# Kernel tuning notes

Measured on AMD Instinct MI355X. Metric: run time of the kernel, lower is better.

## Reference

```python
import jax, jax.numpy as jnp
import numpy as np

L, B, D_IN, D = 96, 32, 4, 128   # leaves, batch, input feats, dim_feedforward
NB, NC = 3, 6                    # n_blocks, n_classes
E = L * (L - 1)                  # directed edges, no self-loops


def _adjacency():
    # one-hot receiver/sender matrices, shape (E, L)
    pairs = np.array([(i, j) for i in range(L) for j in range(L) if i != j])
    recv, send = pairs[:, 0], pairs[:, 1]
    rr = np.zeros((E, L), np.float32); rr[np.arange(E), recv] = 1.0
    rs = np.zeros((E, L), np.float32); rs[np.arange(E), send] = 1.0
    return rr, rs


def setup_inputs() -> dict:
    key = jax.random.key(0)
    ks = jax.random.split(key, 24)
    rr, rs = _adjacency()
    inp = {
        'inputs': jax.random.normal(ks[0], (L, B, D_IN), jnp.float32),
        'rel_rec': jnp.broadcast_to(jnp.asarray(rr), (B, E, L)),
        'rel_send': jnp.broadcast_to(jnp.asarray(rs), (B, E, L)),
    }
    s = 0.1
    # initial MLP: D_IN -> D -> D
    inp['W0a'] = s * jax.random.normal(ks[1], (D_IN, D)); inp['b0a'] = jnp.zeros((D,))
    inp['W0b'] = s * jax.random.normal(ks[2], (D, D));    inp['b0b'] = jnp.zeros((D,))
    # per-block edge MLP (2D -> D -> D) and node MLP (D -> D -> D), stacked over NB
    inp['eW1'] = s * jax.random.normal(ks[3], (NB, 2 * D, D)); inp['eb1'] = jnp.zeros((NB, D))
    inp['eW2'] = s * jax.random.normal(ks[4], (NB, D, D));     inp['eb2'] = jnp.zeros((NB, D))
    inp['nW1'] = s * jax.random.normal(ks[5], (NB, D, D));     inp['nb1'] = jnp.zeros((NB, D))
    inp['nW2'] = s * jax.random.normal(ks[6], (NB, D, D));     inp['nb2'] = jnp.zeros((NB, D))
    # final MLP: 2D -> D -> NC
    inp['fW1'] = s * jax.random.normal(ks[7], (2 * D, D)); inp['fb1'] = jnp.zeros((D,))
    inp['fW2'] = s * jax.random.normal(ks[8], (D, NC));    inp['fb2'] = jnp.zeros((NC,))
    return inp


def _mlp(x, W1, b1, W2, b2):
    return jax.nn.elu(jax.nn.elu(x @ W1 + b1) @ W2 + b2)


def reference(inputs, rel_rec, rel_send, W0a, b0a, W0b, b0b,
              eW1, eb1, eW2, eb2, nW1, nb1, nW2, nb2,
              fW1, fb1, fW2, fb2):
    def node2edge(h):
        # (b,l,d) -> (b,E,2d): cat([senders, receivers])
        senders = jnp.einsum('bel,bld->bed', rel_send, h)
        receivers = jnp.einsum('bel,bld->bed', rel_rec, h)
        return jnp.concatenate([senders, receivers], axis=2)

    def edge2node(h):
        # (b,E,d) -> (b,l,d), mean over incoming edges
        incoming = jnp.einsum('bel,bed->bld', rel_rec, h)
        denom = rel_rec.sum(1)[:, 1]  # (b,)
        return incoming / denom[:, None, None]

    x = jnp.transpose(inputs, (1, 0, 2))           # (b, l, d_in)
    x = _mlp(x, W0a, b0a, W0b, b0b)                # (b, l, D)
    x = node2edge(x)                               # (b, E, 2D)
    for i in range(NB):
        x = _mlp(x, eW1[i], eb1[i], eW2[i], eb2[i])  # (b, E, D)
        x = edge2node(x)                             # (b, l, D)
        x = _mlp(x, nW1[i], nb1[i], nW2[i], nb2[i])  # (b, l, D)
        x = node2edge(x)                             # (b, E, 2D)
    out = jax.nn.elu(x @ fW1 + fb1) @ fW2 + fb2    # (b, E, NC)
    return out
```

## Files before the change

kernel.cpp:

```cpp
#include <hip/hip_runtime.h>
#include <hip/hip_bf16.h>

#define LN 96
#define BN 32
#define DM 128
#define EPN 95

typedef __attribute__((ext_vector_type(8))) short s16x8;
typedef __attribute__((ext_vector_type(4))) float f32x4;

__device__ __forceinline__ float eluf(float x){ return x > 0.f ? x : __expf(x) - 1.f; }
__device__ __forceinline__ unsigned short f2bf(float f){
    unsigned u = __float_as_uint(f);
    return (unsigned short)((u + 0x7fff + ((u >> 16) & 1)) >> 16);
}
__device__ __forceinline__ float bf2f(unsigned short h){ return __uint_as_float(((unsigned)h) << 16); }
__device__ __forceinline__ unsigned cvtpk(float lo, float hi){
    unsigned r;
    asm("v_cvt_pk_bf16_f32 %0, %1, %2" : "=v"(r) : "v"(lo), "v"(hi));
    return r;
}

struct SrcTab { const float* p[19]; };

__global__ void conv_pack_kernel(SrcTab tab, unsigned short* __restrict__ hi,
                                 unsigned short* __restrict__ lo){
    int tid = blockIdx.x * 256 + threadIdx.x;
    int m = tid >> 11, c = tid & 2047;
    int l = c & 63, f = c >> 6;
    int n = (f >> 2) * 16 + (l & 15);
    int k0 = (f & 3) * 32 + (l >> 4) * 8;
    union { unsigned short us[8]; uint4 v; } ph, pl;
#pragma unroll
    for (int e = 0; e < 8; ++e){
        float x;
        if (m == 18) x = (n < 6) ? tab.p[18][(k0 + e) * 6 + n] : 0.f;
        else         x = tab.p[m][(k0 + e) * DM + n];
        unsigned short h = f2bf(x);
        ph.us[e] = h;
        pl.us[e] = f2bf(x - bf2f(h));
    }
    *(uint4*)(hi + (size_t)tid * 8) = ph.v;
    *(uint4*)(lo + (size_t)tid * 8) = pl.v;
}

__device__ __forceinline__ void mmw(const char* atile, int l,
                                    const unsigned short* __restrict__ whW,
                                    const unsigned short* __restrict__ wlW,
                                    f32x4 acc[2]) {
    const int l15 = l & 15, kgrp = l >> 4;
    s16x8 a[4];
#pragma unroll
    for (int ks = 0; ks < 4; ++ks)
        a[ks] = *(const s16x8*)(atile + ((l15 * 256 + (ks * 32 + kgrp * 8) * 2) ^ ((l15 & 7) << 4)));
#pragma unroll
    for (int ntl = 0; ntl < 2; ++ntl) {
#pragma unroll
        for (int ks = 0; ks < 4; ++ks) {
            s16x8 bh = *(const s16x8*)(whW + (size_t)((ntl * 4 + ks) * 64 + l) * 8);
            acc[ntl] = __builtin_amdgcn_mfma_f32_16x16x32_bf16(a[ks], bh, acc[ntl], 0, 0, 0);
        }
#pragma unroll
        for (int ks = 0; ks < 4; ++ks) {
            s16x8 bl = *(const s16x8*)(wlW + (size_t)((ntl * 4 + ks) * 64 + l) * 8);
            acc[ntl] = __builtin_amdgcn_mfma_f32_16x16x32_bf16(a[ks], bl, acc[ntl], 0, 0, 0);
        }
    }
}

__device__ __forceinline__ void store_act(char* atile, int l, int w, f32x4 acc[2]) {
    const int l15 = l & 15, kgrp = l >> 4;
#pragma unroll
    for (int ntl = 0; ntl < 2; ++ntl)
#pragma unroll
        for (int i = 0; i < 4; ++i) {
            int row = kgrp * 4 + i;
            int col = (2 * w + ntl) * 16 + l15;
            *(unsigned short*)(atile + ((row * 256 + col * 2) ^ ((row & 7) << 4))) = f2bf(eluf(acc[ntl][i]));
        }
}

__global__ __launch_bounds__(256) void node0_kernel(
    const float* __restrict__ in,
    const float* __restrict__ W0a, const float* __restrict__ b0a,
    const unsigned short* __restrict__ w2h, const unsigned short* __restrict__ w2l,
    const float* __restrict__ b2,
    const unsigned short* __restrict__ wsh, const unsigned short* __restrict__ wsl,
    const unsigned short* __restrict__ wrh, const unsigned short* __restrict__ wrl,
    const float* __restrict__ bp,
    float* __restrict__ hs, float* __restrict__ hr) {
    __shared__ char atile[16 * 256];
    const int t = threadIdx.x;
    const int q = blockIdx.x >> 5, bblk = blockIdx.x & 31;
    const int row0 = bblk * LN + q * 16;
    const int l = t & 63, w = t >> 6;
    const int l15 = l & 15, kgrp = l >> 4;

    {
        int rr = t >> 4, qq = t & 15, c0 = qq * 8;
        int swz = (rr & 7) << 4;
        union { unsigned short us[8]; uint4 v; } pk;
        int row = row0 + rr;
        int b = row / LN, ll = row - b * LN;
        float4 x = *(const float4*)(in + (size_t)(ll * BN + b) * 4);
#pragma unroll
        for (int j = 0; j < 8; ++j) {
            int cc = c0 + j;
            float a = b0a[cc] + x.x * W0a[cc] + x.y * W0a[DM + cc]
                    + x.z * W0a[2 * DM + cc] + x.w * W0a[3 * DM + cc];
            pk.us[j] = f2bf(eluf(a));
        }
        *(uint4*)(atile + ((rr * 256 + c0 * 2) ^ swz)) = pk.v;
    }
    __syncthreads();

    f32x4 acc[2];
    const int cA = (2 * w) * 16 + l15, cB = (2 * w + 1) * 16 + l15;
    {
        float ba = b2[cA], bb = b2[cB];
        acc[0] = (f32x4){ba, ba, ba, ba};
        acc[1] = (f32x4){bb, bb, bb, bb};
        mmw(atile, l, w2h + w * 4096, w2l + w * 4096, acc);
        __syncthreads();
        store_act(atile, l, w, acc);
        __syncthreads();
    }
    acc[0] = (f32x4){0.f, 0.f, 0.f, 0.f};
    acc[1] = (f32x4){0.f, 0.f, 0.f, 0.f};
    mmw(atile, l, wsh + w * 4096, wsl + w * 4096, acc);
#pragma unroll
    for (int ntl = 0; ntl < 2; ++ntl)
#pragma unroll
        for (int i = 0; i < 4; ++i)
            hs[(size_t)(row0 + kgrp * 4 + i) * DM + (2 * w + ntl) * 16 + l15] = acc[ntl][i];
    {
        float ba = bp[cA], bb = bp[cB];
        acc[0] = (f32x4){ba, ba, ba, ba};
        acc[1] = (f32x4){bb, bb, bb, bb};
        mmw(atile, l, wrh + w * 4096, wrl + w * 4096, acc);
    }
#pragma unroll
    for (int ntl = 0; ntl < 2; ++ntl)
#pragma unroll
        for (int i = 0; i < 4; ++i)
            hr[(size_t)(row0 + kgrp * 4 + i) * DM + (2 * w + ntl) * 16 + l15] = acc[ntl][i];
}

__global__ __launch_bounds__(256) void edge_node_kernel(
    const float* __restrict__ hsIn, const float* __restrict__ hrIn,
    const unsigned short* __restrict__ whi, const unsigned short* __restrict__ wlo,
    int eslot, const float* __restrict__ eb2v,
    int s1, int s2, int sS,
    const float* __restrict__ b1, const float* __restrict__ b2, const float* __restrict__ bp,
    float* __restrict__ hsOut, float* __restrict__ hrOut) {
    __shared__ char y1[LN * 256];
    __shared__ float hrL[6 * DM];
    __shared__ float gL[6 * DM];
    __shared__ char actA[16 * 256];
    __shared__ char actB[16 * 256];
    const int blk = blockIdx.x;
    const int rg = blk >> 5, b = blk & 31;
    const int r0 = rg * 6;
    const int t = threadIdx.x;
    const int w = t >> 6, l = t & 63;
    const int l15 = l & 15, kgrp = l >> 4;

    if (t < 192) {
        int rr = t >> 5, c4 = (t & 31) * 4;
        *(float4*)(hrL + rr * DM + c4) = *(const float4*)(hrIn + ((size_t)(b * LN + r0 + rr)) * DM + c4);
    }
    s16x8 bfr[2][4];
#pragma unroll
    for (int ntl = 0; ntl < 2; ++ntl)
#pragma unroll
        for (int ks = 0; ks < 4; ++ks)
            bfr[ntl][ks] = *(const s16x8*)(whi + (size_t)eslot * 16384 +
                           (size_t)(((2 * w + ntl) * 4 + ks) * 64 + l) * 8);
    float b20 = eb2v[(2 * w) * 16 + l15], b21 = eb2v[(2 * w + 1) * 16 + l15];
    __syncthreads();

    const float* hsB = hsIn + (size_t)(b * LN) * DM;
    for (int rr6 = 0; rr6 < 6; ++rr6) {
        int r = r0 + rr6;
#pragma unroll
        for (int ch = 0; ch < 3; ++ch) {
            float4 h0[2], h1[2];
            int rrs[2], c0s[2];
#pragma unroll
            for (int k = 0; k < 2; ++k) {
                int task = t + (ch * 2 + k) * 256;
                int rr = task >> 4, c0 = (task & 15) * 8;
                rrs[k] = rr; c0s[k] = c0;
                if (rr < EPN) {
                    int j = rr + (rr >= r);
                    const float* hp = hsB + (size_t)j * DM + c0;
                    h0[k] = *(const float4*)hp;
                    h1[k] = *(const float4*)(hp + 4);
                }
            }
#pragma unroll
            for (int k = 0; k < 2; ++k) {
                int rr = rrs[k], c0 = c0s[k];
                int swz = (rr & 7) << 4;
                uint4 pk = make_uint4(0, 0, 0, 0);
                if (rr < EPN) {
                    const float* rp = hrL + rr6 * DM + c0;
                    f32x4 v0 = *(const f32x4*)rp, v1 = *(const f32x4*)(rp + 4);
                    float e0 = eluf(h0[k].x + v0[0]), e1 = eluf(h0[k].y + v0[1]);
                    float e2 = eluf(h0[k].z + v0[2]), e3 = eluf(h0[k].w + v0[3]);
                    float e4 = eluf(h1[k].x + v1[0]), e5 = eluf(h1[k].y + v1[1]);
                    float e6 = eluf(h1[k].z + v1[2]), e7 = eluf(h1[k].w + v1[3]);
                    pk.x = cvtpk(e0, e1); pk.y = cvtpk(e2, e3);
                    pk.z = cvtpk(e4, e5); pk.w = cvtpk(e6, e7);
                }
                *(uint4*)(y1 + ((rr * 256 + c0 * 2) ^ swz)) = pk;
            }
        }
        __syncthreads();
        f32x4 acc[6][2] = {};
#pragma unroll
        for (int mt = 0; mt < 6; ++mt) {
            int arow = mt * 16 + l15;
            const char* rb = y1 + arow * 256;
            int swz = (arow & 7) << 4;
#pragma unroll
            for (int ks = 0; ks < 4; ++ks) {
                s16x8 a = *(const s16x8*)(rb + (((ks * 32 + kgrp * 8) * 2) ^ swz));
                acc[mt][0] = __builtin_amdgcn_mfma_f32_16x16x32_bf16(a, bfr[0][ks], acc[mt][0], 0, 0, 0);
                acc[mt][1] = __builtin_amdgcn_mfma_f32_16x16x32_bf16(a, bfr[1][ks], acc[mt][1], 0, 0, 0);
            }
        }
        float cs0 = 0.f, cs1 = 0.f;
#pragma unroll
        for (int mt = 0; mt < 6; ++mt)
#pragma unroll
            for (int i = 0; i < 4; ++i) {
                int row = mt * 16 + kgrp * 4 + i;
                if (row < EPN) {
                    cs0 += eluf(acc[mt][0][i] + b20);
                    cs1 += eluf(acc[mt][1][i] + b21);
                }
            }
        cs0 += __shfl_xor(cs0, 16); cs0 += __shfl_xor(cs0, 32);
        cs1 += __shfl_xor(cs1, 16); cs1 += __shfl_xor(cs1, 32);
        if (l < 16) {
            gL[rr6 * DM + (2 * w) * 16 + l]     = cs0 * (1.f / 95.f);
            gL[rr6 * DM + (2 * w + 1) * 16 + l] = cs1 * (1.f / 95.f);
        }
        __syncthreads();
    }

    {
        int rr = t >> 4, q = t & 15, c0 = q * 8;
        int swz = (rr & 7) << 4;
        union { unsigned short us[8]; uint4 v; } pk;
        if (rr < 6) {
            const float* src = gL + rr * DM + c0;
            float4 f0 = *(const float4*)(src);
            float4 f1 = *(const float4*)(src + 4);
            pk.us[0] = f2bf(f0.x); pk.us[1] = f2bf(f0.y); pk.us[2] = f2bf(f0.z); pk.us[3] = f2bf(f0.w);
            pk.us[4] = f2bf(f1.x); pk.us[5] = f2bf(f1.y); pk.us[6] = f2bf(f1.z); pk.us[7] = f2bf(f1.w);
        } else pk.v = make_uint4(0, 0, 0, 0);
        *(uint4*)(actA + ((rr * 256 + c0 * 2) ^ swz)) = pk.v;
    }
    __syncthreads();

    f32x4 acc[2];
    const int cA = (2 * w) * 16 + l15, cB = (2 * w + 1) * 16 + l15;
    {
        float ba = b1[cA], bb = b1[cB];
        acc[0] = (f32x4){ba, ba, ba, ba};
        acc[1] = (f32x4){bb, bb, bb, bb};
        mmw(actA, l, whi + (size_t)s1 * 16384 + w * 4096, wlo + (size_t)s1 * 16384 + w * 4096, acc);
        __syncthreads();
        store_act(actB, l, w, acc);
        __syncthreads();
    }
    {
        float ba = b2[cA], bb = b2[cB];
        acc[0] = (f32x4){ba, ba, ba, ba};
        acc[1] = (f32x4){bb, bb, bb, bb};
        mmw(actB, l, whi + (size_t)s2 * 16384 + w * 4096, wlo + (size_t)s2 * 16384 + w * 4096, acc);
        __syncthreads();
        store_act(actA, l, w, acc);
        __syncthreads();
    }
    acc[0] = (f32x4){0.f, 0.f, 0.f, 0.f};
    acc[1] = (f32x4){0.f, 0.f, 0.f, 0.f};
    mmw(actA, l, whi + (size_t)sS * 16384 + w * 4096, wlo + (size_t)sS * 16384 + w * 4096, acc);
#pragma unroll
    for (int ntl = 0; ntl < 2; ++ntl)
#pragma unroll
        for (int i = 0; i < 4; ++i) {
            int row = kgrp * 4 + i;
            if (row < 6)
                hsOut[(size_t)(b * LN + r0 + row) * DM + (2 * w + ntl) * 16 + l15] = acc[ntl][i];
        }
    {
        float ba = bp[cA], bb = bp[cB];
        acc[0] = (f32x4){ba, ba, ba, ba};
        acc[1] = (f32x4){bb, bb, bb, bb};
        mmw(actA, l, whi + (size_t)(sS + 1) * 16384 + w * 4096, wlo + (size_t)(sS + 1) * 16384 + w * 4096, acc);
    }
#pragma unroll
    for (int ntl = 0; ntl < 2; ++ntl)
#pragma unroll
        for (int i = 0; i < 4; ++i) {
            int row = kgrp * 4 + i;
            if (row < 6)
                hrOut[(size_t)(b * LN + r0 + row) * DM + (2 * w + ntl) * 16 + l15] = acc[ntl][i];
        }
}

__global__ void final_kernel(const float* __restrict__ hs, const float* __restrict__ hr,
                             const float* __restrict__ fW2, const float* __restrict__ fb2,
                             float* __restrict__ out) {
    __shared__ float w2l[DM * 6];
    __shared__ float hrbuf[DM];
    const int b = blockIdx.x, r = blockIdx.y;
    const int t = threadIdx.x;
    hrbuf[t] = hr[((size_t)b * LN + r) * DM + t];
    for (int c = 0; c < 6; ++c) w2l[t * 6 + c] = fW2[t * 6 + c];
    __syncthreads();
    int k = t;
    if (k < EPN) {
        int j = k + (k >= r);
        const float* src = hs + ((size_t)b * LN + j) * DM;
        float acc[6];
        for (int c = 0; c < 6; ++c) acc[c] = fb2[c];
        for (int d0 = 0; d0 < DM; d0 += 4) {
            float4 f = *(const float4*)(src + d0);
            float v0 = eluf(f.x + hrbuf[d0 + 0]);
            float v1 = eluf(f.y + hrbuf[d0 + 1]);
            float v2 = eluf(f.z + hrbuf[d0 + 2]);
            float v3 = eluf(f.w + hrbuf[d0 + 3]);
            for (int c = 0; c < 6; ++c)
                acc[c] += v0 * w2l[(d0 + 0) * 6 + c] + v1 * w2l[(d0 + 1) * 6 + c]
                        + v2 * w2l[(d0 + 2) * 6 + c] + v3 * w2l[(d0 + 3) * 6 + c];
        }
        float* o = out + (((size_t)b * (LN * EPN)) + r * EPN + k) * 6;
        for (int c = 0; c < 6; ++c) o[c] = acc[c];
    }
}

extern "C" void kernel_launch(void* const* d_in, const int* in_sizes, int n_in,
                              void* d_out, int out_size, void* d_ws, size_t ws_size,
                              hipStream_t stream) {
    const float* inputs = (const float*)d_in[0];
    const float* W0a = (const float*)d_in[3];
    const float* b0a = (const float*)d_in[4];
    const float* W0b = (const float*)d_in[5];
    const float* b0b = (const float*)d_in[6];
    const float* eW1 = (const float*)d_in[7];
    const float* eb1 = (const float*)d_in[8];
    const float* eW2 = (const float*)d_in[9];
    const float* eb2 = (const float*)d_in[10];
    const float* nW1 = (const float*)d_in[11];
    const float* nb1 = (const float*)d_in[12];
    const float* nW2 = (const float*)d_in[13];
    const float* nb2 = (const float*)d_in[14];
    const float* fW1 = (const float*)d_in[15];
    const float* fb1 = (const float*)d_in[16];
    const float* fW2 = (const float*)d_in[17];
    const float* fb2 = (const float*)d_in[18];
    float* out = (float*)d_out;

    const int NR = BN * LN;
    unsigned short* whi = (unsigned short*)d_ws;
    unsigned short* wlo = whi + 19 * 16384;
    float* hsA = (float*)(wlo + 19 * 16384);
    float* hrA = hsA + NR * DM;
    float* hsB = hrA + NR * DM;
    float* hrB = hsB + NR * DM;

    SrcTab tab;
    tab.p[0] = eW2;          tab.p[1] = eW2 + 16384;  tab.p[2] = eW2 + 32768;
    tab.p[3] = W0b;
    tab.p[4] = eW1;          tab.p[5] = eW1 + 16384;
    tab.p[6] = nW1;          tab.p[7] = nW2;          tab.p[8] = eW1 + 32768;  tab.p[9]  = eW1 + 49152;
    tab.p[10] = nW1 + 16384; tab.p[11] = nW2 + 16384; tab.p[12] = eW1 + 65536; tab.p[13] = eW1 + 81920;
    tab.p[14] = nW1 + 32768; tab.p[15] = nW2 + 32768; tab.p[16] = fW1;         tab.p[17] = fW1 + 16384;
    tab.p[18] = fW2;

    #define WM(m) (whi + (m) * 16384), (wlo + (m) * 16384)

    conv_pack_kernel<<<152, 256, 0, stream>>>(tab, whi, wlo);
    node0_kernel<<<192, 256, 0, stream>>>(inputs, W0a, b0a, WM(3), b0b, WM(4), WM(5), eb1, hsA, hrA);
    edge_node_kernel<<<512, 256, 0, stream>>>(hsA, hrA, whi, wlo, 0, eb2,
                                              6, 7, 8, nb1, nb2, eb1 + DM, hsB, hrB);
    edge_node_kernel<<<512, 256, 0, stream>>>(hsB, hrB, whi, wlo, 1, eb2 + DM,
                                              10, 11, 12, nb1 + DM, nb2 + DM, eb1 + 2 * DM, hsA, hrA);
    edge_node_kernel<<<512, 256, 0, stream>>>(hsA, hrA, whi, wlo, 2, eb2 + 2 * DM,
                                              14, 15, 16, nb1 + 2 * DM, nb2 + 2 * DM, fb1, hsB, hrB);
    final_kernel<<<dim3(BN, LN), 128, 0, stream>>>(hsB, hrB, fW2, fb2, out);
    #undef WM
}
```

Before: 128.8 us.

## Rewrite final edge-MLP output layer as bf16 MFMA over LDS-staged edge tiles

The final kernel now computes the ELU(hs+hr) @ fW2 projection with 16x16x32 bf16 MFMA instructions. It uses split hi/lo bf16 weights from the packed weight buffer, which approximates fp32 precision. Each block handles one batch and six receiver rows. It stages swizzled bf16 activation tiles in LDS, two receivers at a time, instead of one thread per edge doing scalar FMAs with LDS weight reads. This removes the scalar per-thread inner loop at the cost of rounding activations to bf16 and using more LDS per block.

```diff
diff --git a/kernel.cpp b/kernel.cpp
--- a/kernel.cpp
+++ b/kernel.cpp
@@ -312,34 +312,103 @@
         }
 }
 
-__global__ void final_kernel(const float* __restrict__ hs, const float* __restrict__ hr,
-                             const float* __restrict__ fW2, const float* __restrict__ fb2,
-                             float* __restrict__ out) {
-    __shared__ float w2l[DM * 6];
-    __shared__ float hrbuf[DM];
-    const int b = blockIdx.x, r = blockIdx.y;
+__global__ __launch_bounds__(256) void final_kernel(
+    const float* __restrict__ hs, const float* __restrict__ hr,
+    const unsigned short* __restrict__ wfh, const unsigned short* __restrict__ wfl,
+    const float* __restrict__ fb2, float* __restrict__ out) {
+    __shared__ char tA[LN * 256];
+    __shared__ char tB[LN * 256];
+    __shared__ float hrL[6 * DM];
+    const int blk = blockIdx.x;
+    const int rg = blk >> 5, b = blk & 31;
+    const int r0 = rg * 6;
     const int t = threadIdx.x;
-    hrbuf[t] = hr[((size_t)b * LN + r) * DM + t];
-    for (int c = 0; c < 6; ++c) w2l[t * 6 + c] = fW2[t * 6 + c];
+    const int w = t >> 6, l = t & 63;
+    const int l15 = l & 15, kgrp = l >> 4;
+
+    if (t < 192) {
+        int rr = t >> 5, c4 = (t & 31) * 4;
+        *(float4*)(hrL + rr * DM + c4) = *(const float4*)(hr + ((size_t)(b * LN + r0 + rr)) * DM + c4);
+    }
+    s16x8 fh[4], fl4[4];
+#pragma unroll
+    for (int ks = 0; ks < 4; ++ks) {
+        fh[ks]  = *(const s16x8*)(wfh + (size_t)(ks * 64 + l) * 8);
+        fl4[ks] = *(const s16x8*)(wfl + (size_t)(ks * 64 + l) * 8);
+    }
+    float fbv = (l15 < 6) ? fb2[l15] : 0.f;
     __syncthreads();
-    int k = t;
-    if (k < EPN) {
-        int j = k + (k >= r);
-        const float* src = hs + ((size_t)b * LN + j) * DM;
-        float acc[6];
-        for (int c = 0; c < 6; ++c) acc[c] = fb2[c];
-        for (int d0 = 0; d0 < DM; d0 += 4) {
-            float4 f = *(const float4*)(src + d0);
-            float v0 = eluf(f.x + hrbuf[d0 + 0]);
-            float v1 = eluf(f.y + hrbuf[d0 + 1]);
-            float v2 = eluf(f.z + hrbuf[d0 + 2]);
-            float v3 = eluf(f.w + hrbuf[d0 + 3]);
-            for (int c = 0; c < 6; ++c)
-                acc[c] += v0 * w2l[(d0 + 0) * 6 + c] + v1 * w2l[(d0 + 1) * 6 + c]
-                        + v2 * w2l[(d0 + 2) * 6 + c] + v3 * w2l[(d0 + 3) * 6 + c];
-        }
-        float* o = out + (((size_t)b * (LN * EPN)) + r * EPN + k) * 6;
-        for (int c = 0; c < 6; ++c) o[c] = acc[c];
+
+    const float* hsB = hs + (size_t)(b * LN) * DM;
+    for (int pr = 0; pr < 3; ++pr) {
+        const int rA = r0 + pr * 2, rB = rA + 1;
+#pragma unroll
+        for (int ch = 0; ch < 6; ++ch) {
+            float4 h0[2], h1[2];
+            int rrs[2], c0s[2], tts[2];
+#pragma unroll
+            for (int k = 0; k < 2; ++k) {
+                int task = t + (ch * 2 + k) * 256;
+                int tt = task >= 1536;
+                int rem = task - tt * 1536;
+                int rr = rem >> 4, c0 = (rem & 15) * 8;
+                rrs[k] = rr; c0s[k] = c0; tts[k] = tt;
+                if (rr < EPN) {
+                    int r = tt ? rB : rA;
+                    int j = rr + (rr >= r);
+                    const float* hp = hsB + (size_t)j * DM + c0;
+                    h0[k] = *(const float4*)hp;
+                    h1[k] = *(const float4*)(hp + 4);
+                }
+            }
+#pragma unroll
+            for (int k = 0; k < 2; ++k) {
+                int rr = rrs[k], c0 = c0s[k], tt = tts[k];
+                int swz = (rr & 7) << 4;
+                uint4 pk = make_uint4(0, 0, 0, 0);
+                if (rr < EPN) {
+                    const float* rp = hrL + (pr * 2 + tt) * DM + c0;
+                    f32x4 v0 = *(const f32x4*)rp, v1 = *(const f32x4*)(rp + 4);
+                    float e0 = eluf(h0[k].x + v0[0]), e1 = eluf(h0[k].y + v0[1]);
+                    float e2 = eluf(h0[k].z + v0[2]), e3 = eluf(h0[k].w + v0[3]);
+                    float e4 = eluf(h1[k].x + v1[0]), e5 = eluf(h1[k].y + v1[1]);
+                    float e6 = eluf(h1[k].z + v1[2]), e7 = eluf(h1[k].w + v1[3]);
+                    pk.x = cvtpk(e0, e1); pk.y = cvtpk(e2, e3);
+                    pk.z = cvtpk(e4, e5); pk.w = cvtpk(e6, e7);
+                }
+                *(uint4*)((tt ? tB : tA) + ((rr * 256 + c0 * 2) ^ swz)) = pk;
+            }
+        }
+        __syncthreads();
+        for (int q = w; q < 12; q += 4) {
+            int tt = q >= 6;
+            int mt = q - tt * 6;
+            const char* tile = tt ? tB : tA;
+            int r = tt ? rB : rA;
+            int arow = mt * 16 + l15;
+            const char* rb = tile + arow * 256;
+            int swz = (arow & 7) << 4;
+            s16x8 a[4];
+#pragma unroll
+            for (int ks = 0; ks < 4; ++ks)
+                a[ks] = *(const s16x8*)(rb + (((ks * 32 + kgrp * 8) * 2) ^ swz));
+            f32x4 acc = (f32x4){fbv, fbv, fbv, fbv};
+#pragma unroll
+            for (int ks = 0; ks < 4; ++ks)
+                acc = __builtin_amdgcn_mfma_f32_16x16x32_bf16(a[ks], fh[ks], acc, 0, 0, 0);
+#pragma unroll
+            for (int ks = 0; ks < 4; ++ks)
+                acc = __builtin_amdgcn_mfma_f32_16x16x32_bf16(a[ks], fl4[ks], acc, 0, 0, 0);
+            if (l15 < 6) {
+                float* ob = out + ((size_t)b * (LN * EPN) + (size_t)r * EPN) * 6;
+#pragma unroll
+                for (int i = 0; i < 4; ++i) {
+                    int row = mt * 16 + kgrp * 4 + i;
+                    if (row < EPN) ob[(size_t)row * 6 + l15] = acc[i];
+                }
+            }
+        }
+        __syncthreads();
     }
 }
 
@@ -392,6 +461,6 @@
                                               10, 11, 12, nb1 + DM, nb2 + DM, eb1 + 2 * DM, hsA, hrA);
     edge_node_kernel<<<512, 256, 0, stream>>>(hsA, hrA, whi, wlo, 2, eb2 + 2 * DM,
                                               14, 15, 16, nb1 + 2 * DM, nb2 + 2 * DM, fb1, hsB, hrB);
-    final_kernel<<<dim3(BN, LN), 128, 0, stream>>>(hsB, hrB, fW2, fb2, out);
+    final_kernel<<<512, 256, 0, stream>>>(hsB, hrB, WM(18), fb2, out);
     #undef WM
 }
```

Measured after the change: 125.1 us. 2.9% less time.
